# Performance work log

Hardware: AMD Instinct MI355X
Metric: run time of the kernel (lower is better)

The kernel has to match this reference:

```python
import jax, jax.numpy as jnp
import numpy as np

N_NODES = 50000
N_EDGES = 800000
N_GRAPHS = 64
NEG_SLOPE = 0.2  # PyG GATConv leaky_relu default


def gat_conv(x, src, dst, W, a_src, a_dst, b, concat):
    # PyG GATConv (eval mode): h = W x -> [N,H,C]; e_ij = leakyrelu(a_src.h_j + a_dst.h_i)
    # softmax over incoming edges of each dst node; out_i = sum_j alpha_ij h_j
    N = x.shape[0]
    H, C = a_src.shape
    h = (x @ W).reshape(N, H, C)
    score_s = (h * a_src).sum(-1)  # [N,H]
    score_d = (h * a_dst).sum(-1)  # [N,H]
    e = jax.nn.leaky_relu(score_s[src] + score_d[dst], NEG_SLOPE)  # [E,H]
    m = jax.ops.segment_max(e, dst, num_segments=N)  # [N,H]
    ex = jnp.exp(e - m[dst])
    denom = jax.ops.segment_sum(ex, dst, num_segments=N)  # [N,H], >0 due to self loops
    alpha = ex / denom[dst]
    out = jax.ops.segment_sum(h[src] * alpha[..., None], dst, num_segments=N)  # [N,H,C]
    out = out.reshape(N, H * C) if concat else out.mean(axis=1)
    return out + b


def setup_inputs() -> dict:
    key = jax.random.key(0)
    ks = jax.random.split(key, 24)
    d_in, hid, heads, d_out = 16, 64, 4, 10
    hh = hid * heads

    def rn(k, shape, fan_in):
        return jax.random.normal(k, shape, dtype=jnp.float32) / np.sqrt(fan_in)

    inp = {
        "x": jax.random.normal(ks[0], (N_NODES, d_in), dtype=jnp.float32),
        "edge_index": jax.random.randint(ks[1], (2, N_EDGES), 0, N_NODES, dtype=jnp.int32),
        "batch": jnp.sort(jax.random.randint(ks[2], (N_NODES,), 0, N_GRAPHS, dtype=jnp.int32)),
        "A_W": rn(ks[3], (d_in, hid), d_in),
        "A_b": jnp.zeros((hid,), jnp.float32),
        "W0": rn(ks[4], (hid, hh), hid),
        "as0": rn(ks[5], (heads, hid), hid),
        "ad0": rn(ks[6], (heads, hid), hid),
        "b0": jnp.zeros((hh,), jnp.float32),
        "W1": rn(ks[7], (hh, hh), hh),
        "as1": rn(ks[8], (heads, hid), hid),
        "ad1": rn(ks[9], (heads, hid), hid),
        "b1": jnp.zeros((hh,), jnp.float32),
        "W2": rn(ks[10], (hh, hh), hh),
        "as2": rn(ks[11], (heads, hid), hid),
        "ad2": rn(ks[12], (heads, hid), hid),
        "b2": jnp.zeros((hid,), jnp.float32),
        "M0_W": rn(ks[13], (hid, hid), hid),
        "M0_b": jnp.zeros((hid,), jnp.float32),
        "M1_W": rn(ks[14], (hid, d_out), hid),
        "M1_b": jnp.zeros((d_out,), jnp.float32),
    }
    return inp


def reference(x, edge_index, batch, A_W, A_b, W0, as0, ad0, b0, W1, as1, ad1, b1,
              W2, as2, ad2, b2, M0_W, M0_b, M1_W, M1_b):
    N = x.shape[0]
    # sp_agg ('lrgb'): Linear(input_dim, hidden_dim)
    h = x @ A_W + A_b
    # add self loops (PyG GATConv default add_self_loops=True)
    loop = jnp.arange(N, dtype=edge_index.dtype)
    src = jnp.concatenate([edge_index[0], loop])
    dst = jnp.concatenate([edge_index[1], loop])
    # stacked GAT layers; dropout is a no-op at inference
    h = jax.nn.elu(gat_conv(h, src, dst, W0, as0, ad0, b0, concat=True))
    h = jax.nn.elu(gat_conv(h, src, dst, W1, as1, ad1, b1, concat=True))
    h = gat_conv(h, src, dst, W2, as2, ad2, b2, concat=False)
    # global mean pool over graphs
    sums = jax.ops.segment_sum(h, batch, num_segments=N_GRAPHS)
    cnts = jax.ops.segment_sum(jnp.ones((N,), h.dtype), batch, num_segments=N_GRAPHS)
    g = sums / jnp.maximum(cnts, 1.0)[:, None]
    # MLP head: Linear -> ReLU -> Linear (dropout inactive)
    g = jax.nn.relu(g @ M0_W + M0_b)
    return g @ M1_W + M1_b
```

## Files before the change

### kernel.cpp

```cpp
#include <hip/hip_runtime.h>
#include <hip/hip_bf16.h>
#include <hip/hip_fp16.h>

#define NN   50000
#define NE   800000
#define NEP  850000
#define NG   64
#define HH   256
#define DOUT 10
#define SCH  196

typedef __attribute__((ext_vector_type(8))) short bf16x8;
typedef __attribute__((ext_vector_type(4))) float f32x4;

__device__ inline float bf2f(ushort u) {
    union { unsigned int i; float f; } v; v.i = ((unsigned int)u) << 16; return v.f;
}
__device__ inline ushort f2bf(float f) {
    union { float f; unsigned int i; } v; v.f = f;
    unsigned int x = v.i;
    return (ushort)((x + 0x7FFFu + ((x >> 16) & 1u)) >> 16);
}

__global__ __launch_bounds__(256) void k_lin0b(const float* __restrict__ x,
                                               const float* __restrict__ W,
                                               const float* __restrict__ b,
                                               ushort* __restrict__ out) {
    int idx = blockIdx.x * 256 + threadIdx.x;
    int n = idx >> 6, c = idx & 63;
    if (n >= NN) return;
    float acc = b[c];
    #pragma unroll
    for (int k = 0; k < 16; ++k) acc = fmaf(x[n * 16 + k], W[k * 64 + c], acc);
    out[idx] = f2bf(acc);
}

__global__ __launch_bounds__(256) void k_degree(const int* __restrict__ ei, int* __restrict__ deg) {
    int e = blockIdx.x * 256 + threadIdx.x;
    if (e >= NEP) return;
    int dst = (e < NE) ? ei[NE + e] : (e - NE);
    atomicAdd(&deg[dst], 1);
}

__global__ __launch_bounds__(256) void k_scanA(const int* __restrict__ deg, int* __restrict__ bsum) {
    __shared__ int wsum[4];
    int b = blockIdx.x, t = threadIdx.x, lane = t & 63, w = t >> 6;
    int i = b * SCH + t;
    int v = (t < SCH && i < NN) ? deg[i] : 0;
    #pragma unroll
    for (int d = 1; d < 64; d <<= 1) v += __shfl_xor(v, d, 64);
    if (lane == 0) wsum[w] = v;
    __syncthreads();
    if (t == 0) bsum[b] = wsum[0] + wsum[1] + wsum[2] + wsum[3];
}
__global__ __launch_bounds__(256) void k_scanB(const int* __restrict__ bsum,
                                               int* __restrict__ boff,
                                               int* __restrict__ row_ptr) {
    __shared__ int wtot[4];
    int t = threadIdx.x, lane = t & 63, w = t >> 6;
    int v = bsum[t];
    int sc = v;
    #pragma unroll
    for (int d = 1; d < 64; d <<= 1) {
        int u = __shfl_up(sc, (unsigned)d, 64);
        if (lane >= d) sc += u;
    }
    if (lane == 63) wtot[w] = sc;
    __syncthreads();
    int woff = 0;
    #pragma unroll
    for (int k = 0; k < 4; ++k) woff += (k < w) ? wtot[k] : 0;
    boff[t] = woff + sc - v;
    if (t == 0) row_ptr[NN] = NEP;
}
__global__ __launch_bounds__(256) void k_scanC(int* __restrict__ deg,
                                               const int* __restrict__ boff,
                                               int* __restrict__ row_ptr) {
    __shared__ int wtot[4];
    int b = blockIdx.x, t = threadIdx.x, lane = t & 63, w = t >> 6;
    int i = b * SCH + t;
    bool live = (t < SCH && i < NN);
    int v = live ? deg[i] : 0;
    int sc = v;
    #pragma unroll
    for (int d = 1; d < 64; d <<= 1) {
        int u = __shfl_up(sc, (unsigned)d, 64);
        if (lane >= d) sc += u;
    }
    if (lane == 63) wtot[w] = sc;
    __syncthreads();
    int woff = 0;
    #pragma unroll
    for (int k = 0; k < 4; ++k) woff += (k < w) ? wtot[k] : 0;
    if (live) { row_ptr[i] = boff[b] + woff + sc - v; deg[i] = 0; }
}

__global__ __launch_bounds__(256) void k_scatter(const int* __restrict__ ei,
                                                 const int* __restrict__ row_ptr,
                                                 int* __restrict__ cursor,
                                                 int* __restrict__ col_idx) {
    int e = blockIdx.x * 256 + threadIdx.x;
    if (e >= NEP) return;
    int src, dst;
    if (e < NE) { src = ei[e]; dst = ei[NE + e]; }
    else        { src = e - NE; dst = e - NE; }
    int pos = atomicAdd(&cursor[dst], 1);
    col_idx[row_ptr[dst] + pos] = src;
}

template <int K>
__global__ __launch_bounds__(256) void k_wprep(const float* __restrict__ W,
                                               ushort* __restrict__ Whi,
                                               ushort* __restrict__ Wlo) {
    int idx = blockIdx.x * 256 + threadIdx.x;
    int k = idx >> 8, col = idx & 255;
    float v = W[idx];
    ushort hi = f2bf(v);
    Whi[col * K + k] = hi;
    Wlo[col * K + k] = f2bf(v - bf2f(hi));
}

template <int K>
__global__ __launch_bounds__(256) void k_gemm(const ushort* __restrict__ A,
                                              const ushort* __restrict__ Whi,
                                              const ushort* __restrict__ Wlo,
                                              ushort* __restrict__ C,
                                              const float* __restrict__ a_s,
                                              const float* __restrict__ a_d,
                                              float* __restrict__ ss,
                                              float* __restrict__ sd) {
    __shared__ ushort As[64][40];
    __shared__ ushort Bh[256][40];
    __shared__ ushort Bl[256][40];
    int tid = threadIdx.x;
    int w = tid >> 6, l = tid & 63;
    int rl = l & 15, rg = l >> 4;
    int m0 = blockIdx.x * 64;
    f32x4 acc[4][4];
    #pragma unroll
    for (int i = 0; i < 4; ++i)
        #pragma unroll
        for (int j = 0; j < 4; ++j) acc[i][j] = (f32x4){0.f, 0.f, 0.f, 0.f};

    int arow = tid >> 2, ak8 = (tid & 3) << 3;
    for (int k0 = 0; k0 < K; k0 += 32) {
        {
            int gr = m0 + arow; if (gr >= NN) gr = NN - 1;
            *reinterpret_cast<bf16x8*>(&As[arow][ak8]) =
                *reinterpret_cast<const bf16x8*>(&A[gr * K + k0 + ak8]);
        }
        #pragma unroll
        for (int j = 0; j < 4; ++j) {
            *reinterpret_cast<bf16x8*>(&Bh[tid][j << 3]) =
                *reinterpret_cast<const bf16x8*>(&Whi[tid * K + k0 + (j << 3)]);
            *reinterpret_cast<bf16x8*>(&Bl[tid][j << 3]) =
                *reinterpret_cast<const bf16x8*>(&Wlo[tid * K + k0 + (j << 3)]);
        }
        __syncthreads();
        int kg = rg << 3;
        bf16x8 a_frag[4], bh_frag[4], bl_frag[4];
        #pragma unroll
        for (int rt = 0; rt < 4; ++rt)
            a_frag[rt] = *reinterpret_cast<const bf16x8*>(&As[rt * 16 + rl][kg]);
        #pragma unroll
        for (int ct = 0; ct < 4; ++ct) {
            int col = (w << 6) + ct * 16 + rl;
            bh_frag[ct] = *reinterpret_cast<const bf16x8*>(&Bh[col][kg]);
            bl_frag[ct] = *reinterpret_cast<const bf16x8*>(&Bl[col][kg]);
        }
        #pragma unroll
        for (int rt = 0; rt < 4; ++rt)
            #pragma unroll
            for (int ct = 0; ct < 4; ++ct) {
                acc[rt][ct] = __builtin_amdgcn_mfma_f32_16x16x32_bf16(
                    a_frag[rt], bh_frag[ct], acc[rt][ct], 0, 0, 0);
                acc[rt][ct] = __builtin_amdgcn_mfma_f32_16x16x32_bf16(
                    a_frag[rt], bl_frag[ct], acc[rt][ct], 0, 0, 0);
            }
        __syncthreads();
    }
    float as4[4], ad4[4];
    #pragma unroll
    for (int ct = 0; ct < 4; ++ct) {
        as4[ct] = a_s[(w << 6) + ct * 16 + rl];
        ad4[ct] = a_d[(w << 6) + ct * 16 + rl];
    }
    #pragma unroll
    for (int rt = 0; rt < 4; ++rt)
        #pragma unroll
        for (int reg = 0; reg < 4; ++reg) {
            int m = m0 + rt * 16 + (rg << 2) + reg;
            float ps = 0.f, pd = 0.f;
            #pragma unroll
            for (int ct = 0; ct < 4; ++ct) {
                float v = acc[rt][ct][reg];
                ps = fmaf(v, as4[ct], ps);
                pd = fmaf(v, ad4[ct], pd);
                if (m < NN) C[m * HH + (w << 6) + ct * 16 + rl] = f2bf(v);
            }
            #pragma unroll
            for (int d = 1; d < 16; d <<= 1) {
                ps += __shfl_xor(ps, d, 64);
                pd += __shfl_xor(pd, d, 64);
            }
            if (rl == 0 && m < NN) {
                ss[m * 4 + w] = ps;
                sd[m * 4 + w] = pd;
            }
        }
}

__global__ __launch_bounds__(256) void k_alpha(const float* __restrict__ ss,
                                               const float* __restrict__ sd,
                                               const int* __restrict__ row_ptr,
                                               const int* __restrict__ col_idx,
                                               ushort* __restrict__ alp) {
    int wid = threadIdx.x >> 6, lane = threadIdx.x & 63;
    int n = blockIdx.x * 4 + wid;
    int rs = row_ptr[n], re = row_ptr[n + 1];
    float4 sdn = *reinterpret_cast<const float4*>(&sd[n * 4]);
    float m0 = -1e30f, m1 = -1e30f, m2 = -1e30f, m3 = -1e30f;
    float s0 = 0.f, s1 = 0.f, s2 = 0.f, s3 = 0.f;
    for (int e = rs + lane; e < re; e += 64) {
        int sn = col_idx[e];
        float4 t = *reinterpret_cast<const float4*>(&ss[sn * 4]);
        float c0 = t.x + sdn.x; c0 = (c0 > 0.f) ? c0 : 0.2f * c0;
        float c1 = t.y + sdn.y; c1 = (c1 > 0.f) ? c1 : 0.2f * c1;
        float c2 = t.z + sdn.z; c2 = (c2 > 0.f) ? c2 : 0.2f * c2;
        float c3 = t.w + sdn.w; c3 = (c3 > 0.f) ? c3 : 0.2f * c3;
        float mn, d;
        mn = fmaxf(m0, c0); d = __expf(fminf(m0, c0) - mn);
        s0 = (c0 > m0) ? fmaf(s0, d, 1.f) : (s0 + d); m0 = mn;
        mn = fmaxf(m1, c1); d = __expf(fminf(m1, c1) - mn);
        s1 = (c1 > m1) ? fmaf(s1, d, 1.f) : (s1 + d); m1 = mn;
        mn = fmaxf(m2, c2); d = __expf(fminf(m2, c2) - mn);
        s2 = (c2 > m2) ? fmaf(s2, d, 1.f) : (s2 + d); m2 = mn;
        mn = fmaxf(m3, c3); d = __expf(fminf(m3, c3) - mn);
        s3 = (c3 > m3) ? fmaf(s3, d, 1.f) : (s3 + d); m3 = mn;
    }
    #pragma unroll
    for (int dd = 1; dd < 64; dd <<= 1) {
        float mo, so, mn, f;
        mo = __shfl_xor(m0, dd, 64); so = __shfl_xor(s0, dd, 64);
        mn = fmaxf(m0, mo); f = __expf(fminf(m0, mo) - mn);
        s0 = (m0 >= mo) ? fmaf(so, f, s0) : fmaf(s0, f, so); m0 = mn;
        mo = __shfl_xor(m1, dd, 64); so = __shfl_xor(s1, dd, 64);
        mn = fmaxf(m1, mo); f = __expf(fminf(m1, mo) - mn);
        s1 = (m1 >= mo) ? fmaf(so, f, s1) : fmaf(s1, f, so); m1 = mn;
        mo = __shfl_xor(m2, dd, 64); so = __shfl_xor(s2, dd, 64);
        mn = fmaxf(m2, mo); f = __expf(fminf(m2, mo) - mn);
        s2 = (m2 >= mo) ? fmaf(so, f, s2) : fmaf(s2, f, so); m2 = mn;
        mo = __shfl_xor(m3, dd, 64); so = __shfl_xor(s3, dd, 64);
        mn = fmaxf(m3, mo); f = __expf(fminf(m3, mo) - mn);
        s3 = (m3 >= mo) ? fmaf(so, f, s3) : fmaf(s3, f, so); m3 = mn;
    }
    float is0 = 1.f / s0, is1 = 1.f / s1, is2 = 1.f / s2, is3 = 1.f / s3;
    for (int e = rs + lane; e < re; e += 64) {
        int sn = col_idx[e];
        float4 t = *reinterpret_cast<const float4*>(&ss[sn * 4]);
        float c0 = t.x + sdn.x; c0 = (c0 > 0.f) ? c0 : 0.2f * c0;
        float c1 = t.y + sdn.y; c1 = (c1 > 0.f) ? c1 : 0.2f * c1;
        float c2 = t.z + sdn.z; c2 = (c2 > 0.f) ? c2 : 0.2f * c2;
        float c3 = t.w + sdn.w; c3 = (c3 > 0.f) ? c3 : 0.2f * c3;
        ushort4 o;
        o.x = __half_as_ushort(__float2half(__expf(c0 - m0) * is0));
        o.y = __half_as_ushort(__float2half(__expf(c1 - m1) * is1));
        o.z = __half_as_ushort(__float2half(__expf(c2 - m2) * is2));
        o.w = __half_as_ushort(__float2half(__expf(c3 - m3) * is3));
        *reinterpret_cast<ushort4*>(&alp[e * 4]) = o;
    }
}

template <int MODE>
__global__ __launch_bounds__(256) void k_agg(const ushort* __restrict__ hlin,
                                             const ushort* __restrict__ alp,
                                             const int* __restrict__ row_ptr,
                                             const int* __restrict__ col_idx,
                                             const float* __restrict__ bias,
                                             ushort* __restrict__ outb,
                                             float* __restrict__ outf) {
    int wid = threadIdx.x >> 6, lane = threadIdx.x & 63;
    int n = blockIdx.x * 4 + wid;
    int h = lane >> 4, c4 = (lane & 15) << 2;
    int rs = row_ptr[n], re = row_ptr[n + 1];
    float a0 = 0.f, a1 = 0.f, a2 = 0.f, a3 = 0.f;
    int e = rs;
    for (; e + 1 < re; e += 2) {
        int sn0 = col_idx[e], sn1 = col_idx[e + 1];
        float al0 = __half2float(__ushort_as_half(alp[e * 4 + h]));
        float al1 = __half2float(__ushort_as_half(alp[(e + 1) * 4 + h]));
        ushort4 u0 = *reinterpret_cast<const ushort4*>(&hlin[sn0 * HH + (h << 6) + c4]);
        ushort4 u1 = *reinterpret_cast<const ushort4*>(&hlin[sn1 * HH + (h << 6) + c4]);
        a0 = fmaf(al0, bf2f(u0.x), a0);
        a1 = fmaf(al0, bf2f(u0.y), a1);
        a2 = fmaf(al0, bf2f(u0.z), a2);
        a3 = fmaf(al0, bf2f(u0.w), a3);
        a0 = fmaf(al1, bf2f(u1.x), a0);
        a1 = fmaf(al1, bf2f(u1.y), a1);
        a2 = fmaf(al1, bf2f(u1.z), a2);
        a3 = fmaf(al1, bf2f(u1.w), a3);
    }
    if (e < re) {
        int sn0 = col_idx[e];
        float al0 = __half2float(__ushort_as_half(alp[e * 4 + h]));
        ushort4 u0 = *reinterpret_cast<const ushort4*>(&hlin[sn0 * HH + (h << 6) + c4]);
        a0 = fmaf(al0, bf2f(u0.x), a0);
        a1 = fmaf(al0, bf2f(u0.y), a1);
        a2 = fmaf(al0, bf2f(u0.z), a2);
        a3 = fmaf(al0, bf2f(u0.w), a3);
    }
    if (MODE == 0) {
        float o0 = a0 + bias[(h << 6) + c4 + 0];
        float o1 = a1 + bias[(h << 6) + c4 + 1];
        float o2 = a2 + bias[(h << 6) + c4 + 2];
        float o3 = a3 + bias[(h << 6) + c4 + 3];
        o0 = (o0 > 0.f) ? o0 : (__expf(o0) - 1.f);
        o1 = (o1 > 0.f) ? o1 : (__expf(o1) - 1.f);
        o2 = (o2 > 0.f) ? o2 : (__expf(o2) - 1.f);
        o3 = (o3 > 0.f) ? o3 : (__expf(o3) - 1.f);
        ushort4 ob;
        ob.x = f2bf(o0); ob.y = f2bf(o1); ob.z = f2bf(o2); ob.w = f2bf(o3);
        *reinterpret_cast<ushort4*>(&outb[n * HH + (h << 6) + c4]) = ob;
    } else {
        a0 += __shfl_xor(a0, 16, 64); a0 += __shfl_xor(a0, 32, 64);
        a1 += __shfl_xor(a1, 16, 64); a1 += __shfl_xor(a1, 32, 64);
        a2 += __shfl_xor(a2, 16, 64); a2 += __shfl_xor(a2, 32, 64);
        a3 += __shfl_xor(a3, 16, 64); a3 += __shfl_xor(a3, 32, 64);
        if (h == 0) {
            float4 o = make_float4(0.25f * a0 + bias[c4 + 0],
                                   0.25f * a1 + bias[c4 + 1],
                                   0.25f * a2 + bias[c4 + 2],
                                   0.25f * a3 + bias[c4 + 3]);
            *reinterpret_cast<float4*>(&outf[n * 64 + c4]) = o;
        }
    }
}

__global__ __launch_bounds__(256) void k_poolG(const float* __restrict__ h,
                                               const int* __restrict__ batch,
                                               float* __restrict__ pool) {
    __shared__ float part[4][64];
    int g = blockIdx.x;
    int lo = 0, hi = NN;
    while (lo < hi) { int mid = (lo + hi) >> 1; if (batch[mid] < g) lo = mid + 1; else hi = mid; }
    int s = lo;
    lo = 0; hi = NN;
    while (lo < hi) { int mid = (lo + hi) >> 1; if (batch[mid] < g + 1) lo = mid + 1; else hi = mid; }
    int e = lo;
    int c = threadIdx.x & 63, r = threadIdx.x >> 6;
    float acc = 0.f;
    for (int n = s + r; n < e; n += 4) acc += h[n * 64 + c];
    part[r][c] = acc;
    __syncthreads();
    if (r == 0) {
        float v = part[0][c] + part[1][c] + part[2][c] + part[3][c];
        pool[g * 64 + c] = v / fmaxf((float)(e - s), 1.f);
    }
}

__global__ __launch_bounds__(256) void k_mlp(const float* __restrict__ pool,
                                             const float* __restrict__ M0W,
                                             const float* __restrict__ M0b,
                                             const float* __restrict__ M1W,
                                             const float* __restrict__ M1b,
                                             float* __restrict__ out) {
    __shared__ float g[64][64];
    __shared__ float t1[64][64];
    int tid = threadIdx.x;
    for (int idx = tid; idx < 4096; idx += 256) {
        g[idx >> 6][idx & 63] = pool[idx];
    }
    __syncthreads();
    for (int idx = tid; idx < 4096; idx += 256) {
        int i = idx >> 6, j = idx & 63;
        float acc = M0b[j];
        for (int k = 0; k < 64; ++k) acc = fmaf(g[i][k], M0W[k * 64 + j], acc);
        t1[i][j] = fmaxf(acc, 0.f);
    }
    __syncthreads();
    for (int idx = tid; idx < NG * DOUT; idx += 256) {
        int i = idx / DOUT, j = idx % DOUT;
        float acc = M1b[j];
        for (int k = 0; k < 64; ++k) acc = fmaf(t1[i][k], M1W[k * DOUT + j], acc);
        out[idx] = acc;
    }
}

extern "C" void kernel_launch(void* const* d_in, const int* in_sizes, int n_in,
                              void* d_out, int out_size, void* d_ws, size_t ws_size,
                              hipStream_t stream) {
    const float* x   = (const float*)d_in[0];
    const int*   ei  = (const int*)d_in[1];
    const int*   bat = (const int*)d_in[2];
    const float* A_W = (const float*)d_in[3];
    const float* A_b = (const float*)d_in[4];
    const float* W0  = (const float*)d_in[5];
    const float* as0 = (const float*)d_in[6];
    const float* ad0 = (const float*)d_in[7];
    const float* b0  = (const float*)d_in[8];
    const float* W1  = (const float*)d_in[9];
    const float* as1 = (const float*)d_in[10];
    const float* ad1 = (const float*)d_in[11];
    const float* b1  = (const float*)d_in[12];
    const float* W2  = (const float*)d_in[13];
    const float* as2 = (const float*)d_in[14];
    const float* ad2 = (const float*)d_in[15];
    const float* b2  = (const float*)d_in[16];
    const float* M0W = (const float*)d_in[17];
    const float* M0b = (const float*)d_in[18];
    const float* M1W = (const float*)d_in[19];
    const float* M1b = (const float*)d_in[20];

    char* ws = (char*)d_ws;
    ushort* hB_bf   = (ushort*)(ws);
    ushort* hA_bf   = (ushort*)(ws + 25600000);
    ushort* h0_bf   = (ushort*)(ws + 51200000);
    float*  h2      = (float*) (ws + 57600000);
    float*  ss      = (float*) (ws + 70400000);
    float*  sd      = (float*) (ws + 71200000);
    int*    row_ptr = (int*)   (ws + 72000000);
    int*    cursor  = (int*)   (ws + 72200064);
    int*    col_idx = (int*)   (ws + 72400128);
    float*  pool    = (float*) (ws + 75800128);
    ushort* Whi     = (ushort*)(ws + 75817536);
    ushort* Wlo     = (ushort*)(ws + 75948608);
    int*    bsum    = (int*)   (ws + 76079680);
    int*    boff    = (int*)   (ws + 76080704);
    ushort* alp     = (ushort*)(ws + 76081728);

    const int EB = (NEP + 255) / 256;
    const int GB = (NN + 63) / 64;

    k_lin0b<<<(NN * 64) / 256, 256, 0, stream>>>(x, A_W, A_b, h0_bf);

    hipMemsetAsync(cursor, 0, NN * sizeof(int), stream);
    k_degree<<<EB, 256, 0, stream>>>(ei, cursor);
    k_scanA<<<256, 256, 0, stream>>>(cursor, bsum);
    k_scanB<<<1, 256, 0, stream>>>(bsum, boff, row_ptr);
    k_scanC<<<256, 256, 0, stream>>>(cursor, boff, row_ptr);
    k_scatter<<<EB, 256, 0, stream>>>(ei, row_ptr, cursor, col_idx);

    k_wprep<64><<<64, 256, 0, stream>>>(W0, Whi, Wlo);
    k_gemm<64><<<GB, 256, 0, stream>>>(h0_bf, Whi, Wlo, hB_bf, as0, ad0, ss, sd);
    k_alpha<<<12500, 256, 0, stream>>>(ss, sd, row_ptr, col_idx, alp);
    k_agg<0><<<12500, 256, 0, stream>>>(hB_bf, alp, row_ptr, col_idx, b0, hA_bf, nullptr);
    k_wprep<256><<<256, 256, 0, stream>>>(W1, Whi, Wlo);
    k_gemm<256><<<GB, 256, 0, stream>>>(hA_bf, Whi, Wlo, hB_bf, as1, ad1, ss, sd);
    k_alpha<<<12500, 256, 0, stream>>>(ss, sd, row_ptr, col_idx, alp);
    k_agg<0><<<12500, 256, 0, stream>>>(hB_bf, alp, row_ptr, col_idx, b1, hA_bf, nullptr);
    k_wprep<256><<<256, 256, 0, stream>>>(W2, Whi, Wlo);
    k_gemm<256><<<GB, 256, 0, stream>>>(hA_bf, Whi, Wlo, hB_bf, as2, ad2, ss, sd);
    k_alpha<<<12500, 256, 0, stream>>>(ss, sd, row_ptr, col_idx, alp);
    k_agg<1><<<12500, 256, 0, stream>>>(hB_bf, alp, row_ptr, col_idx, b2, nullptr, h2);

    k_poolG<<<NG, 256, 0, stream>>>(h2, bat, pool);
    k_mlp<<<1, 256, 0, stream>>>(pool, M0W, M0b, M1W, M1b, (float*)d_out);
}
```

Measured before the change: 693.7 us.

## Split GAT aggregation per head across blocks, fold final head-mean into pooling

Aggregation now assigns one head per block: each lane loads a single bf16 element instead of a ushort4 covering four heads, and blocks are interleaved so the four heads of a node chunk run together, which is meant to improve cache locality on the gathered rows. For the last layer, per-head bf16 partials are written out and the head mean plus bias is folded into the pooling kernel, removing the shuffle reduction. The trade-off is four times as many blocks with narrower 2-byte loads, plus bf16 rounding of the final layer outputs before pooling.

After: 1.040 ms. 1.5x slower.

```diff
diff --git a/kernel.cpp b/kernel.cpp
--- a/kernel.cpp
+++ b/kernel.cpp
@@ -272,72 +272,49 @@
 }
 
 template <int MODE>
-__global__ __launch_bounds__(256) void k_agg(const ushort* __restrict__ hlin,
-                                             const ushort* __restrict__ alp,
-                                             const int* __restrict__ row_ptr,
-                                             const int* __restrict__ col_idx,
-                                             const float* __restrict__ bias,
-                                             ushort* __restrict__ outb,
-                                             float* __restrict__ outf) {
-    int wid = threadIdx.x >> 6, lane = threadIdx.x & 63;
-    int n = blockIdx.x * 4 + wid;
-    int h = lane >> 4, c4 = (lane & 15) << 2;
+__global__ __launch_bounds__(256) void k_aggH(const ushort* __restrict__ hlin,
+                                              const ushort* __restrict__ alp,
+                                              const int* __restrict__ row_ptr,
+                                              const int* __restrict__ col_idx,
+                                              const float* __restrict__ bias,
+                                              ushort* __restrict__ outb,
+                                              ushort* __restrict__ hp) {
+    int b = blockIdx.x;
+    int x = b & 7;
+    int head = x & 3;
+    int chunk = (b >> 3) * 2 + (x >> 2);
+    int wid = threadIdx.x >> 6, l = threadIdx.x & 63;
+    int n = chunk * 4 + wid;
     int rs = row_ptr[n], re = row_ptr[n + 1];
-    float a0 = 0.f, a1 = 0.f, a2 = 0.f, a3 = 0.f;
+    int hoff = (head << 6) + l;
+    float a = 0.f;
     int e = rs;
     for (; e + 1 < re; e += 2) {
         int sn0 = col_idx[e], sn1 = col_idx[e + 1];
-        float al0 = __half2float(__ushort_as_half(alp[e * 4 + h]));
-        float al1 = __half2float(__ushort_as_half(alp[(e + 1) * 4 + h]));
-        ushort4 u0 = *reinterpret_cast<const ushort4*>(&hlin[sn0 * HH + (h << 6) + c4]);
-        ushort4 u1 = *reinterpret_cast<const ushort4*>(&hlin[sn1 * HH + (h << 6) + c4]);
-        a0 = fmaf(al0, bf2f(u0.x), a0);
-        a1 = fmaf(al0, bf2f(u0.y), a1);
-        a2 = fmaf(al0, bf2f(u0.z), a2);
-        a3 = fmaf(al0, bf2f(u0.w), a3);
-        a0 = fmaf(al1, bf2f(u1.x), a0);
-        a1 = fmaf(al1, bf2f(u1.y), a1);
-        a2 = fmaf(al1, bf2f(u1.z), a2);
-        a3 = fmaf(al1, bf2f(u1.w), a3);
+        float al0 = __half2float(__ushort_as_half(alp[e * 4 + head]));
+        float al1 = __half2float(__ushort_as_half(alp[(e + 1) * 4 + head]));
+        float v0 = bf2f(hlin[sn0 * HH + hoff]);
+        float v1 = bf2f(hlin[sn1 * HH + hoff]);
+        a = fmaf(al0, v0, a);
+        a = fmaf(al1, v1, a);
     }
     if (e < re) {
-        int sn0 = col_idx[e];
-        float al0 = __half2float(__ushort_as_half(alp[e * 4 + h]));
-        ushort4 u0 = *reinterpret_cast<const ushort4*>(&hlin[sn0 * HH + (h << 6) + c4]);
-        a0 = fmaf(al0, bf2f(u0.x), a0);
-        a1 = fmaf(al0, bf2f(u0.y), a1);
-        a2 = fmaf(al0, bf2f(u0.z), a2);
-        a3 = fmaf(al0, bf2f(u0.w), a3);
+        int sn = col_idx[e];
+        float al = __half2float(__ushort_as_half(alp[e * 4 + head]));
+        a = fmaf(al, bf2f(hlin[sn * HH + hoff]), a);
     }
     if (MODE == 0) {
-        float o0 = a0 + bias[(h << 6) + c4 + 0];
-        float o1 = a1 + bias[(h << 6) + c4 + 1];
-        float o2 = a2 + bias[(h << 6) + c4 + 2];
-        float o3 = a3 + bias[(h << 6) + c4 + 3];
-        o0 = (o0 > 0.f) ? o0 : (__expf(o0) - 1.f);
-        o1 = (o1 > 0.f) ? o1 : (__expf(o1) - 1.f);
-        o2 = (o2 > 0.f) ? o2 : (__expf(o2) - 1.f);
-        o3 = (o3 > 0.f) ? o3 : (__expf(o3) - 1.f);
-        ushort4 ob;
-        ob.x = f2bf(o0); ob.y = f2bf(o1); ob.z = f2bf(o2); ob.w = f2bf(o3);
-        *reinterpret_cast<ushort4*>(&outb[n * HH + (h << 6) + c4]) = ob;
+        float o = a + bias[hoff];
+        o = (o > 0.f) ? o : (__expf(o) - 1.f);
+        outb[n * HH + hoff] = f2bf(o);
     } else {
-        a0 += __shfl_xor(a0, 16, 64); a0 += __shfl_xor(a0, 32, 64);
-        a1 += __shfl_xor(a1, 16, 64); a1 += __shfl_xor(a1, 32, 64);
-        a2 += __shfl_xor(a2, 16, 64); a2 += __shfl_xor(a2, 32, 64);
-        a3 += __shfl_xor(a3, 16, 64); a3 += __shfl_xor(a3, 32, 64);
-        if (h == 0) {
-            float4 o = make_float4(0.25f * a0 + bias[c4 + 0],
-                                   0.25f * a1 + bias[c4 + 1],
-                                   0.25f * a2 + bias[c4 + 2],
-                                   0.25f * a3 + bias[c4 + 3]);
-            *reinterpret_cast<float4*>(&outf[n * 64 + c4]) = o;
-        }
-    }
-}
-
-__global__ __launch_bounds__(256) void k_poolG(const float* __restrict__ h,
+        hp[head * (NN * 64) + n * 64 + l] = f2bf(a);
+    }
+}
+
+__global__ __launch_bounds__(256) void k_poolG(const ushort* __restrict__ hp,
                                                const int* __restrict__ batch,
+                                               const float* __restrict__ b2,
                                                float* __restrict__ pool) {
     __shared__ float part[4][64];
     int g = blockIdx.x;
@@ -349,12 +326,15 @@
     int e = lo;
     int c = threadIdx.x & 63, r = threadIdx.x >> 6;
     float acc = 0.f;
-    for (int n = s + r; n < e; n += 4) acc += h[n * 64 + c];
+    for (int n = s + r; n < e; n += 4) {
+        acc += bf2f(hp[0 * NN * 64 + n * 64 + c]) + bf2f(hp[1 * NN * 64 + n * 64 + c])
+             + bf2f(hp[2 * NN * 64 + n * 64 + c]) + bf2f(hp[3 * NN * 64 + n * 64 + c]);
+    }
     part[r][c] = acc;
     __syncthreads();
     if (r == 0) {
-        float v = part[0][c] + part[1][c] + part[2][c] + part[3][c];
-        pool[g * 64 + c] = v / fmaxf((float)(e - s), 1.f);
+        float v = 0.25f * (part[0][c] + part[1][c] + part[2][c] + part[3][c]);
+        pool[g * 64 + c] = v / fmaxf((float)(e - s), 1.f) + b2[c];
     }
 }
 
@@ -414,8 +394,8 @@
     char* ws = (char*)d_ws;
     ushort* hB_bf   = (ushort*)(ws);
     ushort* hA_bf   = (ushort*)(ws + 25600000);
+    ushort* hp      = (ushort*)(ws + 25600000);
     ushort* h0_bf   = (ushort*)(ws + 51200000);
-    float*  h2      = (float*) (ws + 57600000);
     float*  ss      = (float*) (ws + 70400000);
     float*  sd      = (float*) (ws + 71200000);
     int*    row_ptr = (int*)   (ws + 72000000);
@@ -430,6 +410,7 @@
 
     const int EB = (NEP + 255) / 256;
     const int GB = (NN + 63) / 64;
+    const int AB = 50000;
 
     k_lin0b<<<(NN * 64) / 256, 256, 0, stream>>>(x, A_W, A_b, h0_bf);
 
@@ -443,16 +424,16 @@
     k_wprep<64><<<64, 256, 0, stream>>>(W0, Whi, Wlo);
     k_gemm<64><<<GB, 256, 0, stream>>>(h0_bf, Whi, Wlo, hB_bf, as0, ad0, ss, sd);
     k_alpha<<<12500, 256, 0, stream>>>(ss, sd, row_ptr, col_idx, alp);
-    k_agg<0><<<12500, 256, 0, stream>>>(hB_bf, alp, row_ptr, col_idx, b0, hA_bf, nullptr);
+    k_aggH<0><<<AB, 256, 0, stream>>>(hB_bf, alp, row_ptr, col_idx, b0, hA_bf, nullptr);
     k_wprep<256><<<256, 256, 0, stream>>>(W1, Whi, Wlo);
     k_gemm<256><<<GB, 256, 0, stream>>>(hA_bf, Whi, Wlo, hB_bf, as1, ad1, ss, sd);
     k_alpha<<<12500, 256, 0, stream>>>(ss, sd, row_ptr, col_idx, alp);
-    k_agg<0><<<12500, 256, 0, stream>>>(hB_bf, alp, row_ptr, col_idx, b1, hA_bf, nullptr);
+    k_aggH<0><<<AB, 256, 0, stream>>>(hB_bf, alp, row_ptr, col_idx, b1, hA_bf, nullptr);
     k_wprep<256><<<256, 256, 0, stream>>>(W2, Whi, Wlo);
     k_gemm<256><<<GB, 256, 0, stream>>>(hA_bf, Whi, Wlo, hB_bf, as2, ad2, ss, sd);
     k_alpha<<<12500, 256, 0, stream>>>(ss, sd, row_ptr, col_idx, alp);
-    k_agg<1><<<12500, 256, 0, stream>>>(hB_bf, alp, row_ptr, col_idx, b2, nullptr, h2);
-
-    k_poolG<<<NG, 256, 0, stream>>>(h2, bat, pool);
+    k_aggH<1><<<AB, 256, 0, stream>>>(hB_bf, alp, row_ptr, col_idx, nullptr, nullptr, hp);
+
+    k_poolG<<<NG, 256, 0, stream>>>(hp, bat, b2, pool);
     k_mlp<<<1, 256, 0, stream>>>(pool, M0W, M0b, M1W, M1b, (float*)d_out);
 }
```
